# Kernel optimization log

Hardware: AMD Instinct MI355X
Metric: run time of the kernel (lower is better)

The kernel has to match this reference:

```python
import jax, jax.numpy as jnp
import numpy as np

D_MODEL = 1024
D_STATE = 16
D_CONV = 4
EXPAND = 2
D_INNER = D_MODEL * EXPAND
BATCH = 4
SEQ_LEN = 4096


def setup_inputs() -> dict:
    key = jax.random.key(0)
    ks = jax.random.split(key, 6)
    def rn(k, shape, scale):
        return jax.random.normal(k, shape, dtype=jnp.float32) * scale
    x = rn(ks[0], (BATCH, SEQ_LEN, D_MODEL), 1.0)
    in_proj_w = rn(ks[1], (2 * D_INNER, D_MODEL), D_MODEL ** -0.5)
    conv_w = rn(ks[2], (D_INNER, 1, D_CONV), D_CONV ** -0.5)  # depthwise conv kernel
    conv_b = rn(ks[3], (D_INNER,), 0.02)
    x_proj_w = rn(ks[4], (2 * D_STATE + 1, D_INNER), D_INNER ** -0.5)
    A_log = jnp.log(jnp.arange(1, D_STATE + 1, dtype=jnp.float32))  # module's init
    D = jnp.ones((D_INNER,), jnp.float32)
    out_proj_w = rn(ks[5], (D_MODEL, D_INNER), D_INNER ** -0.5)
    return dict(x=x, in_proj_w=in_proj_w, conv_w=conv_w, conv_b=conv_b,
                x_proj_w=x_proj_w, A_log=A_log, D=D, out_proj_w=out_proj_w)


def _silu(v):
    return v * jax.nn.sigmoid(v)


def reference(x, in_proj_w, conv_w, conv_b, x_proj_w, A_log, D, out_proj_w):
    b, l, _ = x.shape
    # input projection -> (b, l, 2*d_inner), split into x_inner and gate z
    xz = jnp.einsum('bld,ed->ble', x, in_proj_w)
    x_inner, z = jnp.split(xz, 2, axis=-1)
    # causal depthwise conv1d: torch pads both sides d_conv-1 then truncates to l,
    # equivalent to left-pad d_conv-1 only
    xc = jnp.transpose(x_inner, (0, 2, 1))  # (b, d_inner, l)
    xc = jax.lax.conv_general_dilated(
        xc, conv_w, window_strides=(1,), padding=[(D_CONV - 1, 0)],
        feature_group_count=D_INNER, dimension_numbers=('NCH', 'OIH', 'NCH'))
    xc = xc + conv_b[None, :, None]
    x_conv = _silu(jnp.transpose(xc, (0, 2, 1)))  # (b, l, d_inner)
    # SSM parameter projection: [delta(1) | B(d_state) | C(d_state)]
    x_dbl = jnp.einsum('bld,ed->ble', x_conv, x_proj_w)
    delta = jax.nn.softplus(x_dbl[..., 0])       # (b, l) scalar per token
    B_ssm = x_dbl[..., 1:D_STATE + 1]            # (b, l, n)
    C_ssm = x_dbl[..., D_STATE + 1:]             # (b, l, n)
    A = -jnp.exp(A_log)                          # (n,)

    def step(h, inp):
        x_t, d_t, B_t, C_t = inp  # (b,d_inner), (b,), (b,n), (b,n)
        dA = jnp.exp(d_t[:, None, None] * A)          # (b, 1, n)
        dB = d_t[:, None, None] * B_t[:, None, :]     # (b, 1, n)
        h = h * dA + x_t[:, :, None] * dB             # (b, d_inner, n)
        y_t = jnp.einsum('bdn,bn->bd', h, C_t)
        return h, y_t

    h0 = jnp.zeros((b, D_INNER, D_STATE), x.dtype)
    xs = (jnp.swapaxes(x_conv, 0, 1), jnp.swapaxes(delta, 0, 1),
          jnp.swapaxes(B_ssm, 0, 1), jnp.swapaxes(C_ssm, 0, 1))
    _, ys = jax.lax.scan(step, h0, xs)  # ys: (l, b, d_inner)
    y = jnp.swapaxes(ys, 0, 1)
    y = y + x_conv * D
    y = y * _silu(z)
    return jnp.einsum('bld,od->blo', y, out_proj_w)
```

## Files before the change

### kernel.cpp

```cpp
#include <hip/hip_runtime.h>
#include <hip/hip_fp16.h>

typedef _Float16 f16;
typedef _Float16 half8 __attribute__((ext_vector_type(8)));
typedef _Float16 half4v __attribute__((ext_vector_type(4)));
typedef float f32x4 __attribute__((ext_vector_type(4)));

#define AS1(p) ((const __attribute__((address_space(1))) void*)(p))
#define AS3(p) ((__attribute__((address_space(3))) void*)(p))

__device__ __forceinline__ void gload_lds16(const void* g, void* l) {
    __builtin_amdgcn_global_load_lds(AS1(g), AS3(l), 16, 0, 0);
}

__global__ __launch_bounds__(256)
void prep_k(const float* __restrict__ x, const float* __restrict__ w_in,
            const float* __restrict__ w_xp, const float* __restrict__ w_out,
            f16* __restrict__ xh, f16* __restrict__ wih,
            f16* __restrict__ Wh, f16* __restrict__ woh) {
    int b = blockIdx.x;
    if (b < 2048) {
        for (int i = b * 256 + threadIdx.x; i < 4194304; i += 2048 * 256) {
            float4 v = ((const float4*)x)[i];
            half4v o; o[0] = (f16)v.x; o[1] = (f16)v.y; o[2] = (f16)v.z; o[3] = (f16)v.w;
            ((half4v*)xh)[i] = o;
        }
    } else if (b < 2560) {
        for (int i = (b - 2048) * 256 + threadIdx.x; i < 1048576; i += 512 * 256) {
            float4 v = ((const float4*)w_in)[i];
            half4v o; o[0] = (f16)v.x; o[1] = (f16)v.y; o[2] = (f16)v.z; o[3] = (f16)v.w;
            ((half4v*)wih)[i] = o;
        }
    } else if (b < 2944) {
        int idx = (b - 2560) * 256 + threadIdx.x;
        int e = idx >> 11;
        int k = idx & 2047;
        Wh[idx] = (e < 33) ? (f16)w_xp[e * 2048 + k] : (f16)0.f;
    } else {
        for (int i = (b - 2944) * 256 + threadIdx.x; i < 524288; i += 512 * 256) {
            float4 v = ((const float4*)w_out)[i];
            half4v o; o[0] = (f16)v.x; o[1] = (f16)v.y; o[2] = (f16)v.z; o[3] = (f16)v.w;
            ((half4v*)woh)[i] = o;
        }
    }
}

__device__ __forceinline__ void stage_q(const f16* __restrict__ g, int ld,
                                        int row0, int gk, f16* q,
                                        int tid, int wave) {
#pragma unroll
    for (int rd = 0; rd < 2; ++rd) {
        int t = rd * 512 + tid;
        int r = t >> 2;
        int cu = (t & 3) ^ ((r >> 1) & 3);
        gload_lds16(g + (size_t)(row0 + r) * ld + gk + cu * 8,
                    q + rd * 4096 + wave * 512);
    }
}

#define PH(Q, KH, MH, LOADB, STAGE, WAITC)                                    \
  {                                                                           \
    half8 afr[4];                                                             \
    {                                                                         \
      const f16* aq = &lds[Q][0][KH][0];                                      \
      int ra = wm * 128 + (MH) * 64 + lr;                                     \
      afr[0] = *(const half8*)(aq + (ra +  0) * 32 + cofs);                   \
      afr[1] = *(const half8*)(aq + (ra + 16) * 32 + cofs);                   \
      afr[2] = *(const half8*)(aq + (ra + 32) * 32 + cofs);                   \
      afr[3] = *(const half8*)(aq + (ra + 48) * 32 + cofs);                   \
    }                                                                         \
    if (LOADB) {                                                              \
      const f16* bq = &lds[Q][1][KH][0];                                      \
      int rb = wn * 64 + lr;                                                  \
      bfr[0] = *(const half8*)(bq + (rb +  0) * 32 + cofs);                   \
      bfr[1] = *(const half8*)(bq + (rb + 16) * 32 + cofs);                   \
      bfr[2] = *(const half8*)(bq + (rb + 32) * 32 + cofs);                   \
      bfr[3] = *(const half8*)(bq + (rb + 48) * 32 + cofs);                   \
    }                                                                         \
    STAGE;                                                                    \
    __builtin_amdgcn_s_barrier();                                             \
    asm volatile("s_waitcnt lgkmcnt(0)" ::: "memory");                        \
    __builtin_amdgcn_sched_barrier(0);                                        \
    __builtin_amdgcn_s_setprio(1);                                            \
    _Pragma("unroll")                                                         \
    for (int f_ = 0; f_ < 4; ++f_)                                            \
      _Pragma("unroll")                                                       \
      for (int j_ = 0; j_ < 4; ++j_)                                          \
        acc[(MH) * 4 + f_][j_] = __builtin_amdgcn_mfma_f32_16x16x32_f16(      \
            afr[f_], bfr[j_], acc[(MH) * 4 + f_][j_], 0, 0, 0);               \
    __builtin_amdgcn_s_setprio(0);                                            \
    __builtin_amdgcn_sched_barrier(0);                                        \
    WAITC;                                                                    \
    __builtin_amdgcn_s_barrier();                                             \
  }

template <typename OutT, int NT>
__global__ __launch_bounds__(512, 2)
void gemm8p_pers(const f16* __restrict__ A, const f16* __restrict__ B,
                 OutT* __restrict__ C, int N, int K, int lda, int ldc) {
    __shared__ f16 lds[2][2][2][8192];

    int nTn = N >> 8;
    unsigned grid = gridDim.x;
    unsigned cpx = (grid * (unsigned)NT) >> 3;

    int tid = threadIdx.x;
    int wave = tid >> 6;
    int lane = tid & 63;
    int wm = wave >> 2;
    int wn = wave & 3;
    int lr = lane & 15;
    int cg = lane >> 4;
    int cofs = ((cg ^ ((lr >> 1) & 3)) << 3);

    f32x4 acc[8][4];
#pragma unroll
    for (int i = 0; i < 8; ++i)
#pragma unroll
        for (int j = 0; j < 4; ++j) acc[i][j] = (f32x4){0.f, 0.f, 0.f, 0.f};
    half8 bfr[4];

    auto tileMN = [&](int j, int& tm, int& tn) {
        unsigned o = blockIdx.x + grid * (unsigned)j;
        unsigned s = (o & 7u) * cpx + (o >> 3);
        unsigned gnn = (unsigned)(4 * nTn);
        unsigned g = s / gnn;
        unsigned r = s - g * gnn;
        tm = (int)(g * 4 + (r & 3u)) * 256;
        tn = (int)(r >> 2) * 256;
    };

    int bm, bn;
    tileMN(0, bm, bn);

    stage_q(B, K,   bn, 0,  &lds[0][1][0][0], tid, wave);
    stage_q(A, lda, bm, 0,  &lds[0][0][0][0], tid, wave);
    stage_q(B, K,   bn, 32, &lds[0][1][1][0], tid, wave);
    stage_q(A, lda, bm, 32, &lds[0][0][1][0], tid, wave);
    stage_q(B, K,   bn, 64, &lds[1][1][0][0], tid, wave);
    stage_q(A, lda, bm, 64, &lds[1][0][0][0], tid, wave);
    stage_q(B, K,   bn, 96, &lds[1][1][1][0], tid, wave);
    asm volatile("s_waitcnt vmcnt(6)" ::: "memory");
    __builtin_amdgcn_s_barrier();

    int NI = K >> 7;
    for (int j = 0; j < NT; ++j) {
        int bm2 = bm, bn2 = bn;
        if (j + 1 < NT) tileMN(j + 1, bm2, bn2);

        for (int it = 0; it < NI; ++it) {
            int gk = it << 7;
            bool lastIter = (it == NI - 1);
            bool fin = lastIter && (j + 1 == NT);
            int sbm = lastIter ? bm2 : bm;
            int sbn = lastIter ? bn2 : bn;
            int sgk = lastIter ? 0 : gk + 128;

            PH(0, 0, 0, true,
               { stage_q(A, lda, bm, gk + 96, &lds[1][0][1][0], tid, wave); }, {});
            PH(0, 0, 1, false,
               { if (!fin) stage_q(B, K, sbn, sgk, &lds[0][1][0][0], tid, wave); }, {});
            PH(0, 1, 0, true,
               { if (!fin) stage_q(A, lda, sbm, sgk, &lds[0][0][0][0], tid, wave); }, {});
            PH(0, 1, 1, false,
               { if (!fin) stage_q(B, K, sbn, sgk + 32, &lds[0][1][1][0], tid, wave); },
               { if (fin) asm volatile("s_waitcnt vmcnt(0)" ::: "memory");
                 else     asm volatile("s_waitcnt vmcnt(6)" ::: "memory"); });
            PH(1, 0, 0, true,
               { if (!fin) stage_q(A, lda, sbm, sgk + 32, &lds[0][0][1][0], tid, wave); }, {});
            PH(1, 0, 1, false,
               { if (!fin) stage_q(B, K, sbn, sgk + 64, &lds[1][1][0][0], tid, wave); }, {});
            PH(1, 1, 0, true,
               { if (!fin) stage_q(A, lda, sbm, sgk + 64, &lds[1][0][0][0], tid, wave); }, {});
            PH(1, 1, 1, false,
               { if (!fin) stage_q(B, K, sbn, sgk + 96, &lds[1][1][1][0], tid, wave); },
               { if (!fin) asm volatile("s_waitcnt vmcnt(6)" ::: "memory"); });
        }

        int orow0 = bm + wm * 128 + (lane >> 4) * 4;
        int ocol0 = bn + wn * 64 + lr;
#pragma unroll
        for (int mf = 0; mf < 8; ++mf)
#pragma unroll
            for (int nj = 0; nj < 4; ++nj)
#pragma unroll
                for (int r = 0; r < 4; ++r)
                    C[(size_t)(orow0 + mf * 16 + r) * ldc + (ocol0 + nj * 16)] =
                        (OutT)acc[mf][nj][r];
#pragma unroll
        for (int i2 = 0; i2 < 8; ++i2)
#pragma unroll
            for (int j2 = 0; j2 < 4; ++j2) acc[i2][j2] = (f32x4){0.f, 0.f, 0.f, 0.f};
        bm = bm2; bn = bn2;
    }
}

__global__ __launch_bounds__(256, 2)
void xdbl_mfma_k(const f16* __restrict__ xc, const f16* __restrict__ Wh,
                 float* __restrict__ xdbl) {
    __shared__ f16 As[64 * 64];
    __shared__ f16 Bs[48 * 64];
    int bm = blockIdx.x * 64;
    int tid = threadIdx.x;
    int wave = tid >> 6;
    int lane = tid & 63;
    int srow = lane >> 3;
    int scol = (lane & 7) * 8;
    int lr = lane & 15;
    int lkh = (lane >> 4) * 8;

    f32x4 acc[3];
#pragma unroll
    for (int j = 0; j < 3; ++j) acc[j] = (f32x4){0.f, 0.f, 0.f, 0.f};

    for (int k0 = 0; k0 < 2048; k0 += 64) {
        __syncthreads();
#pragma unroll
        for (int i = 0; i < 2; ++i) {
            int slot = wave * 2 + i;
            gload_lds16(xc + (size_t)(bm + slot * 8 + srow) * 2048 + (k0 + scol),
                        As + slot * 512);
        }
        if (wave < 3) {
#pragma unroll
            for (int i = 0; i < 2; ++i) {
                int slot = wave * 2 + i;
                gload_lds16(Wh + (size_t)(slot * 8 + srow) * 2048 + (k0 + scol),
                            Bs + slot * 512);
            }
        }
        asm volatile("s_waitcnt vmcnt(0)" ::: "memory");
        __syncthreads();
#pragma unroll
        for (int kk = 0; kk < 2; ++kk) {
            half8 a = *(const half8*)(As + (wave * 16 + lr) * 64 + kk * 32 + lkh);
#pragma unroll
            for (int nj = 0; nj < 3; ++nj) {
                half8 b = *(const half8*)(Bs + (nj * 16 + lr) * 64 + kk * 32 + lkh);
                acc[nj] = __builtin_amdgcn_mfma_f32_16x16x32_f16(a, b, acc[nj], 0, 0, 0);
            }
        }
    }

    int orow0 = bm + wave * 16 + (lane >> 4) * 4;
#pragma unroll
    for (int nj = 0; nj < 3; ++nj) {
        int col = nj * 16 + lr;
        if (col < 33) {
#pragma unroll
            for (int r = 0; r < 4; ++r)
                xdbl[(size_t)(orow0 + r) * 33 + col] = acc[nj][r];
        }
    }
}

__global__ __launch_bounds__(256)
void conv_silu_k(const f16* __restrict__ xz, const float* __restrict__ cw,
                 const float* __restrict__ cb, f16* __restrict__ xc) {
    int r0 = blockIdx.x * 8;
    int d0 = threadIdx.x << 3;
    int l0 = r0 & 4095;

    const float4* cw4 = (const float4*)cw;
    float4 w[8];
    float bias[8];
#pragma unroll
    for (int e = 0; e < 8; ++e) { w[e] = cw4[d0 + e]; bias[e] = cb[d0 + e]; }

    half8 xv[11];
#pragma unroll
    for (int j = 0; j < 11; ++j) {
        if (l0 - 3 + j >= 0)
            xv[j] = *(const half8*)(xz + (size_t)(r0 - 3 + j) * 4096 + d0);
        else
            xv[j] = (half8){};
    }

#pragma unroll
    for (int rr = 0; rr < 8; ++rr) {
        float acc[8];
#pragma unroll
        for (int e = 0; e < 8; ++e) acc[e] = bias[e];
#pragma unroll
        for (int k = 0; k < 4; ++k) {
            half8 xk = xv[rr + k];
#pragma unroll
            for (int e = 0; e < 8; ++e) {
                float wj = (k == 0) ? w[e].x : (k == 1) ? w[e].y : (k == 2) ? w[e].z : w[e].w;
                acc[e] = fmaf((float)xk[e], wj, acc[e]);
            }
        }
        half8 out = {};
#pragma unroll
        for (int e = 0; e < 8; ++e) {
            float v = acc[e];
            out[e] = (f16)(v / (1.f + expf(-v)));
        }
        *(half8*)(xc + (size_t)(r0 + rr) * 2048 + d0) = out;
    }
}

__device__ __forceinline__ void build_sp(const float* __restrict__ xdbl,
                                         const float* __restrict__ alog,
                                         float* sp, float* red,
                                         int bc, int tid) {
    if (tid < 128) {
        int m = bc * 128 + tid;
        const float* row = xdbl + (size_t)m * 33;
        float v0 = row[0];
        float d = (v0 > 15.f) ? v0 : logf(1.f + expf(v0));
        float* s = sp + tid * 48;
#pragma unroll
        for (int n = 0; n < 16; ++n) {
            float An = -expf(alog[n]);
            s[n] = expf(An * d);
            s[16 + n] = d * row[1 + n];
            s[32 + n] = row[17 + n];
        }
        if (red) red[tid] = d;
    }
}

__global__ __launch_bounds__(256)
void scan1_k(const f16* __restrict__ xc, const float* __restrict__ xdbl,
             const float* __restrict__ A_log,
             f16* __restrict__ F, float* __restrict__ G) {
    __shared__ float sp[128 * 48];
    __shared__ float red[128];
    __shared__ float alog[16];
    int blk = blockIdx.x;
    int dg = blk & 7;
    int bc = blk >> 3;
    int tid = threadIdx.x;
    int d = dg * 256 + tid;
    int mbase = bc * 128;

    if (tid < 16) alog[tid] = A_log[tid];
    __syncthreads();
    build_sp(xdbl, alog, sp, red, bc, tid);
    __syncthreads();
#pragma unroll
    for (int s2 = 64; s2 > 0; s2 >>= 1) {
        if (tid < s2) red[tid] += red[tid + s2];
        __syncthreads();
    }
    if (dg == 0 && tid < 16)
        G[bc * 16 + tid] = expf(-expf(alog[tid]) * red[0]);

    float h[16];
#pragma unroll
    for (int n = 0; n < 16; ++n) h[n] = 0.f;

#pragma unroll 2
    for (int tt = 0; tt < 128; ++tt) {
        const float* r = sp + tt * 48;
        float x = (float)xc[(size_t)(mbase + tt) * 2048 + d];
#pragma unroll
        for (int n = 0; n < 16; ++n) h[n] = fmaf(h[n], r[n], x * r[16 + n]);
    }
    size_t fb = ((size_t)bc * 2048 + d) * 16;
    half8 o0, o1;
#pragma unroll
    for (int n = 0; n < 8; ++n) { o0[n] = (f16)h[n]; o1[n] = (f16)h[8 + n]; }
    *(half8*)(F + fb) = o0;
    *(half8*)(F + fb + 8) = o1;
}

__global__ __launch_bounds__(256)
void combine_k(const f16* __restrict__ F, const float* __restrict__ G,
               f16* __restrict__ H0) {
    int gid = blockIdx.x * 256 + threadIdx.x;
    int b = gid >> 15;
    int dn = gid & 32767;
    int n = dn & 15;
    float h = 0.f;
    for (int c = 0; c < 32; ++c) {
        int bc = b * 32 + c;
        size_t idx = (size_t)bc * 32768 + dn;
        H0[idx] = (f16)h;
        h = fmaf(G[bc * 16 + n], h, (float)F[idx]);
    }
}

__global__ __launch_bounds__(256)
void scan2_k(const f16* __restrict__ xc, const f16* xz,
             const float* __restrict__ xdbl, const float* __restrict__ A_log,
             const f16* __restrict__ H0, const float* __restrict__ Dv,
             f16* yout) {
    __shared__ float sp[128 * 48];
    __shared__ float alog[16];
    int blk = blockIdx.x;
    int dg = blk & 7;
    int bc = blk >> 3;
    int tid = threadIdx.x;
    int d = dg * 256 + tid;
    int mbase = bc * 128;

    if (tid < 16) alog[tid] = A_log[tid];
    __syncthreads();
    build_sp(xdbl, alog, sp, nullptr, bc, tid);
    __syncthreads();

    size_t fb = ((size_t)bc * 2048 + d) * 16;
    half8 v0 = *(const half8*)(H0 + fb);
    half8 v1 = *(const half8*)(H0 + fb + 8);
    float h[16];
#pragma unroll
    for (int n = 0; n < 8; ++n) { h[n] = (float)v0[n]; h[8 + n] = (float)v1[n]; }
    float Dd = Dv[d];

#pragma unroll 2
    for (int tt = 0; tt < 128; ++tt) {
        const float* r = sp + tt * 48;
        size_t mrow = (size_t)(mbase + tt);
        float x = (float)xc[mrow * 2048 + d];
        float z = (float)xz[mrow * 4096 + 2048 + d];
        float y0 = 0.f, y1 = 0.f, y2 = 0.f, y3 = 0.f;
#pragma unroll
        for (int n = 0; n < 16; n += 4) {
            h[n]     = fmaf(h[n],     r[n],     x * r[16 + n]);
            h[n + 1] = fmaf(h[n + 1], r[n + 1], x * r[17 + n]);
            h[n + 2] = fmaf(h[n + 2], r[n + 2], x * r[18 + n]);
            h[n + 3] = fmaf(h[n + 3], r[n + 3], x * r[19 + n]);
            y0 = fmaf(h[n],     r[32 + n], y0);
            y1 = fmaf(h[n + 1], r[33 + n], y1);
            y2 = fmaf(h[n + 2], r[34 + n], y2);
            y3 = fmaf(h[n + 3], r[35 + n], y3);
        }
        float y = (y0 + y1) + (y2 + y3);
        float yf = fmaf(x, Dd, y);
        float sz = z / (1.f + expf(-z));
        yout[mrow * 4096 + d] = (f16)(yf * sz);
    }
}

extern "C" void kernel_launch(void* const* d_in, const int* in_sizes, int n_in,
                              void* d_out, int out_size, void* d_ws, size_t ws_size,
                              hipStream_t stream) {
    const float* x      = (const float*)d_in[0];
    const float* w_in   = (const float*)d_in[1];
    const float* conv_w = (const float*)d_in[2];
    const float* conv_b = (const float*)d_in[3];
    const float* w_xp   = (const float*)d_in[4];
    const float* A_log  = (const float*)d_in[5];
    const float* Dv     = (const float*)d_in[6];
    const float* w_out  = (const float*)d_in[7];

    char* base = (char*)d_ws;
    f16* xzh = (f16*)base;
    char* r1 = base + 134217728;
    f16* xh  = (f16*)r1;
    f16* wih = (f16*)(r1 + 33554432);
    f16* xch = (f16*)r1;
    char* p = base + 201326592;
    float* xdbl = (float*)p;  p += 2162688;
    float* G    = (float*)p;  p += 8192;
    f16*   F    = (f16*)p;    p += 8388608;
    f16*   H0   = (f16*)p;    p += 8388608;
    f16*   Wh   = (f16*)p;    p += 196608;
    f16*   woh  = (f16*)p;    p += 4194304;

    prep_k<<<3456, 256, 0, stream>>>(x, w_in, w_xp, w_out, xh, wih, Wh, woh);

    gemm8p_pers<f16, 4><<<256, 512, 0, stream>>>(xh, wih, xzh, 4096, 1024, 1024, 4096);

    conv_silu_k<<<2048, 256, 0, stream>>>(xzh, conv_w, conv_b, xch);

    xdbl_mfma_k<<<256, 256, 0, stream>>>(xch, Wh, xdbl);

    scan1_k<<<1024, 256, 0, stream>>>(xch, xdbl, A_log, F, G);
    combine_k<<<512, 256, 0, stream>>>(F, G, H0);
    scan2_k<<<1024, 256, 0, stream>>>(xch, xzh, xdbl, A_log, H0, Dv, xzh);

    gemm8p_pers<float, 1><<<256, 512, 0, stream>>>(xzh, woh, (float*)d_out,
                                                   1024, 2048, 4096, 1024);
}
```

Measured before the change: 434.1 us.

## Split x_proj GEMM along K into four slices and sum partials in scan prologue

The x_proj MFMA kernel previously launched only 256 blocks, each looping over the full K=2048, which leaves much of a large GPU idle. It now launches 1024 blocks, each covering a 512-wide K slice and writing its own partial output buffer. The scan kernels add the four partials when building their per-chunk parameters. This costs a larger workspace and four times the xdbl reads in both scan kernels. Separately, the GEMM macro drops an explicit lgkmcnt wait and sched_barrier before the MFMA block, leaving the compiler to insert the LDS waits itself.

```diff
diff --git a/kernel.cpp b/kernel.cpp
--- a/kernel.cpp
+++ b/kernel.cpp
@@ -79,8 +79,6 @@
     }                                                                         \
     STAGE;                                                                    \
     __builtin_amdgcn_s_barrier();                                             \
-    asm volatile("s_waitcnt lgkmcnt(0)" ::: "memory");                        \
-    __builtin_amdgcn_sched_barrier(0);                                        \
     __builtin_amdgcn_s_setprio(1);                                            \
     _Pragma("unroll")                                                         \
     for (int f_ = 0; f_ < 4; ++f_)                                            \
@@ -197,10 +195,13 @@
 
 __global__ __launch_bounds__(256, 2)
 void xdbl_mfma_k(const f16* __restrict__ xc, const f16* __restrict__ Wh,
-                 float* __restrict__ xdbl) {
+                 float* __restrict__ xdbl4) {
     __shared__ f16 As[64 * 64];
     __shared__ f16 Bs[48 * 64];
-    int bm = blockIdx.x * 64;
+    int blk = blockIdx.x;
+    int bm = (blk & 255) * 64;
+    int slice = blk >> 8;
+    int kbase = slice * 512;
     int tid = threadIdx.x;
     int wave = tid >> 6;
     int lane = tid & 63;
@@ -213,7 +214,7 @@
 #pragma unroll
     for (int j = 0; j < 3; ++j) acc[j] = (f32x4){0.f, 0.f, 0.f, 0.f};
 
-    for (int k0 = 0; k0 < 2048; k0 += 64) {
+    for (int k0 = kbase; k0 < kbase + 512; k0 += 64) {
         __syncthreads();
 #pragma unroll
         for (int i = 0; i < 2; ++i) {
@@ -242,6 +243,7 @@
         }
     }
 
+    float* out = xdbl4 + (size_t)slice * 540672;
     int orow0 = bm + wave * 16 + (lane >> 4) * 4;
 #pragma unroll
     for (int nj = 0; nj < 3; ++nj) {
@@ -249,7 +251,7 @@
         if (col < 33) {
 #pragma unroll
             for (int r = 0; r < 4; ++r)
-                xdbl[(size_t)(orow0 + r) * 33 + col] = acc[nj][r];
+                out[(size_t)(orow0 + r) * 33 + col] = acc[nj][r];
         }
     }
 }
@@ -300,29 +302,34 @@
     }
 }
 
-__device__ __forceinline__ void build_sp(const float* __restrict__ xdbl,
+__device__ __forceinline__ void build_sp(const float* __restrict__ xdbl4,
                                          const float* __restrict__ alog,
                                          float* sp, float* red,
                                          int bc, int tid) {
     if (tid < 128) {
         int m = bc * 128 + tid;
-        const float* row = xdbl + (size_t)m * 33;
-        float v0 = row[0];
+        const float* r0 = xdbl4 + (size_t)m * 33;
+        const float* r1 = r0 + 540672;
+        const float* r2 = r1 + 540672;
+        const float* r3 = r2 + 540672;
+        float v0 = ((r0[0] + r1[0]) + (r2[0] + r3[0]));
         float d = (v0 > 15.f) ? v0 : logf(1.f + expf(v0));
         float* s = sp + tid * 48;
 #pragma unroll
         for (int n = 0; n < 16; ++n) {
             float An = -expf(alog[n]);
+            float Bn = (r0[1 + n] + r1[1 + n]) + (r2[1 + n] + r3[1 + n]);
+            float Cn = (r0[17 + n] + r1[17 + n]) + (r2[17 + n] + r3[17 + n]);
             s[n] = expf(An * d);
-            s[16 + n] = d * row[1 + n];
-            s[32 + n] = row[17 + n];
+            s[16 + n] = d * Bn;
+            s[32 + n] = Cn;
         }
         if (red) red[tid] = d;
     }
 }
 
 __global__ __launch_bounds__(256)
-void scan1_k(const f16* __restrict__ xc, const float* __restrict__ xdbl,
+void scan1_k(const f16* __restrict__ xc, const float* __restrict__ xdbl4,
              const float* __restrict__ A_log,
              f16* __restrict__ F, float* __restrict__ G) {
     __shared__ float sp[128 * 48];
@@ -337,7 +344,7 @@
 
     if (tid < 16) alog[tid] = A_log[tid];
     __syncthreads();
-    build_sp(xdbl, alog, sp, red, bc, tid);
+    build_sp(xdbl4, alog, sp, red, bc, tid);
     __syncthreads();
 #pragma unroll
     for (int s2 = 64; s2 > 0; s2 >>= 1) {
@@ -384,7 +391,7 @@
 
 __global__ __launch_bounds__(256)
 void scan2_k(const f16* __restrict__ xc, const f16* xz,
-             const float* __restrict__ xdbl, const float* __restrict__ A_log,
+             const float* __restrict__ xdbl4, const float* __restrict__ A_log,
              const f16* __restrict__ H0, const float* __restrict__ Dv,
              f16* yout) {
     __shared__ float sp[128 * 48];
@@ -398,7 +405,7 @@
 
     if (tid < 16) alog[tid] = A_log[tid];
     __syncthreads();
-    build_sp(xdbl, alog, sp, nullptr, bc, tid);
+    build_sp(xdbl4, alog, sp, nullptr, bc, tid);
     __syncthreads();
 
     size_t fb = ((size_t)bc * 2048 + d) * 16;
@@ -453,7 +460,7 @@
     f16* wih = (f16*)(r1 + 33554432);
     f16* xch = (f16*)r1;
     char* p = base + 201326592;
-    float* xdbl = (float*)p;  p += 2162688;
+    float* xdbl4 = (float*)p; p += 8650752;
     float* G    = (float*)p;  p += 8192;
     f16*   F    = (f16*)p;    p += 8388608;
     f16*   H0   = (f16*)p;    p += 8388608;
@@ -466,11 +473,11 @@
 
     conv_silu_k<<<2048, 256, 0, stream>>>(xzh, conv_w, conv_b, xch);
 
-    xdbl_mfma_k<<<256, 256, 0, stream>>>(xch, Wh, xdbl);
-
-    scan1_k<<<1024, 256, 0, stream>>>(xch, xdbl, A_log, F, G);
+    xdbl_mfma_k<<<1024, 256, 0, stream>>>(xch, Wh, xdbl4);
+
+    scan1_k<<<1024, 256, 0, stream>>>(xch, xdbl4, A_log, F, G);
     combine_k<<<512, 256, 0, stream>>>(F, G, H0);
-    scan2_k<<<1024, 256, 0, stream>>>(xch, xzh, xdbl, A_log, H0, Dv, xzh);
+    scan2_k<<<1024, 256, 0, stream>>>(xch, xzh, xdbl4, A_log, H0, Dv, xzh);
 
     gemm8p_pers<float, 1><<<256, 512, 0, stream>>>(xzh, woh, (float*)d_out,
                                                    1024, 2048, 4096, 1024);
```

Result: slower. 492.8 us (+13.5%).
